# Performance work log

Hardware: AMD Instinct MI355X
Metric: run time of the kernel (lower is better)

Reference implementation:

```python
import jax, jax.numpy as jnp
import numpy as np

NEG_MASK_SCALE = -1e-09  # faithful to source (source uses -1e-09, likely intended -1e9)


def setup_inputs() -> dict:
    key0 = jax.random.key(0)
    ks = jax.random.split(key0, 7)
    B, Q, K, H = 4, 256, 1024, 128
    return {
        "query": jax.random.normal(ks[0], (B, Q, H), dtype=jnp.float32),
        "key": jax.random.normal(ks[1], (B, K, H), dtype=jnp.float32),
        "value": jax.random.normal(ks[2], (B, K, H), dtype=jnp.float32),
        "mask": jax.random.randint(ks[3], (B, Q, K), 0, 2).astype(jnp.int32),
        "Wq": jax.random.normal(ks[4], (H, H), dtype=jnp.float32) * (1.0 / np.sqrt(H)),
        "Wk": jax.random.normal(ks[5], (H, H), dtype=jnp.float32) * (1.0 / np.sqrt(H)),
        "v": jax.random.normal(ks[6], (H,), dtype=jnp.float32) * (1.0 / np.sqrt(H)),
    }


def reference(query, key, value, mask, Wq, Wk, v):
    # Projections: torch Linear computes x @ W.T
    q_proj = jnp.einsum("bqd,hd->bqh", query, Wq)  # (B, Q, H)
    k_proj = jnp.einsum("bkd,hd->bkh", key, Wk)    # (B, K, H)
    # Additive (Bahdanau) score: v . tanh(q_proj[:, :, None] + k_proj[:, None])
    feat = jnp.tanh(q_proj[:, :, None, :] + k_proj[:, None, :, :])  # (B, Q, K, H)
    score = jnp.einsum("bqkh,h->bqk", feat, v)                      # (B, Q, K)
    score = score + NEG_MASK_SCALE * (1.0 - mask.astype(score.dtype))
    attention_weights = jax.nn.softmax(score, axis=-1)              # (B, Q, K)
    context_vector = jnp.einsum("bqk,bkv->bqv", attention_weights, value)  # (B, Q, V)
    return attention_weights, context_vector
```

## Files before the change

### kernel.cpp

```cpp
#include <hip/hip_runtime.h>

#define Bb 4
#define Qn 256
#define Kn 1024
#define Hn 128

constexpr float SCALE = 2.88539008177792681f;

#if __has_builtin(__builtin_amdgcn_exp2f)
#define EXP2F(x) __builtin_amdgcn_exp2f(x)
#else
#define EXP2F(x) exp2f(x)
#endif
#if __has_builtin(__builtin_amdgcn_rcpf)
#define RCPF(x) __builtin_amdgcn_rcpf(x)
#else
#define RCPF(x) (1.0f / (x))
#endif

__global__ __launch_bounds__(128) void proj_kernel(const float* __restrict__ query,
                                                   const float* __restrict__ key,
                                                   const float* __restrict__ Wq,
                                                   const float* __restrict__ Wk,
                                                   float* __restrict__ eq,
                                                   float* __restrict__ ekT) {
    __shared__ float4 xs[128];
    const int tid = threadIdx.x;
    const bool isQ = blockIdx.x < (Bb * Qn / 4);
    const int r0 = (isQ ? blockIdx.x : blockIdx.x - Bb * Qn / 4) * 4;
    const float* x = isQ ? query : key;
    const float* W = isQ ? Wq : Wk;

    xs[tid] = ((const float4*)(x + (size_t)r0 * Hn))[tid];
    __syncthreads();
    const float4* W4 = (const float4*)W + (size_t)tid * (Hn / 4);
    float acc0 = 0.f, acc1 = 0.f, acc2 = 0.f, acc3 = 0.f;
#pragma unroll 8
    for (int d = 0; d < Hn / 4; ++d) {
        float4 w = W4[d];
        float4 a0 = xs[d];
        float4 a1 = xs[32 + d];
        float4 a2 = xs[64 + d];
        float4 a3 = xs[96 + d];
        acc0 = fmaf(w.x, a0.x, fmaf(w.y, a0.y, fmaf(w.z, a0.z, fmaf(w.w, a0.w, acc0))));
        acc1 = fmaf(w.x, a1.x, fmaf(w.y, a1.y, fmaf(w.z, a1.z, fmaf(w.w, a1.w, acc1))));
        acc2 = fmaf(w.x, a2.x, fmaf(w.y, a2.y, fmaf(w.z, a2.z, fmaf(w.w, a2.w, acc2))));
        acc3 = fmaf(w.x, a3.x, fmaf(w.y, a3.y, fmaf(w.z, a3.z, fmaf(w.w, a3.w, acc3))));
    }
    if (isQ) {
        eq[(size_t)(r0 + 0) * Hn + tid] = EXP2F(acc0 * SCALE);
        eq[(size_t)(r0 + 1) * Hn + tid] = EXP2F(acc1 * SCALE);
        eq[(size_t)(r0 + 2) * Hn + tid] = EXP2F(acc2 * SCALE);
        eq[(size_t)(r0 + 3) * Hn + tid] = EXP2F(acc3 * SCALE);
    } else {
        const int b = r0 / Kn;
        const int k0 = r0 % Kn;
        float4 res = make_float4(EXP2F(acc0 * SCALE), EXP2F(acc1 * SCALE),
                                 EXP2F(acc2 * SCALE), EXP2F(acc3 * SCALE));
        ((float4*)ekT)[((size_t)b * Hn + tid) * (Kn / 4) + (k0 >> 2)] = res;
    }
}

__global__ __launch_bounds__(1024) void score_softmax_kernel(const float* __restrict__ eq,
                                                             const float* __restrict__ ekT,
                                                             const float* __restrict__ v,
                                                             float* __restrict__ attn) {
    const int k = threadIdx.x;
    const int q = blockIdx.x;
    const int b = blockIdx.y;

    __shared__ float red[16][2];

    const float* eqrow = eq + ((size_t)b * Qn + q) * Hn;
    const float* ekb = ekT + (size_t)b * Hn * Kn + k;

    float a = 0.f;
#pragma unroll 16
    for (int h = 0; h < Hn; ++h) {
        const float qe = eqrow[h];
        const float vh = v[h];
        const float kv = ekb[(size_t)h * Kn];
        const float r = RCPF(fmaf(qe, kv, 1.0f));
        a = fmaf(vh, r, a);
    }

    const int lane = k & 63, wv = k >> 6;
    float mn = a;
#pragma unroll
    for (int off = 32; off; off >>= 1) mn = fminf(mn, __shfl_xor(mn, off));
    if (lane == 0) red[wv][0] = mn;
    __syncthreads();
    mn = red[0][0];
#pragma unroll
    for (int w = 1; w < 16; ++w) mn = fminf(mn, red[w][0]);

    const float e = EXP2F((mn - a) * SCALE);
    float s = e;
#pragma unroll
    for (int off = 32; off; off >>= 1) s += __shfl_xor(s, off);
    if (lane == 0) red[wv][1] = s;
    __syncthreads();
    s = red[0][1];
#pragma unroll
    for (int w = 1; w < 16; ++w) s += red[w][1];

    attn[((size_t)b * Qn + q) * Kn + k] = e * RCPF(s);
}

__global__ __launch_bounds__(1024) void ctx_kernel(const float* __restrict__ attn,
                                                   const float* __restrict__ value,
                                                   float* __restrict__ ctx) {
    const int tid = threadIdx.x;
    const int q0 = blockIdx.x * 4;
    const int b = blockIdx.y;

    __shared__ __align__(16) float4 pl[8][4][Hn / 4];

    const int kc = tid >> 7;
    const int cq = (tid >> 5) & 3;
    const int h4 = tid & 31;
    const float4* vb = (const float4*)(value + ((size_t)b * Kn + kc * 128) * Hn) + h4;
    const float* wr = attn + ((size_t)b * Qn + q0 + cq) * Kn + kc * 128;
    float4 acc = make_float4(0.f, 0.f, 0.f, 0.f);
#pragma unroll 4
    for (int kk = 0; kk < 128; ++kk) {
        const float wgt = wr[kk];
        const float4 vv = vb[(size_t)kk * (Hn / 4)];
        acc.x = fmaf(wgt, vv.x, acc.x);
        acc.y = fmaf(wgt, vv.y, acc.y);
        acc.z = fmaf(wgt, vv.z, acc.z);
        acc.w = fmaf(wgt, vv.w, acc.w);
    }
    pl[kc][cq][h4] = acc;
    __syncthreads();
    if (tid < 128) {
        const int q = tid >> 5, h = tid & 31;
        float4 r0 = pl[0][q][h], r1 = pl[1][q][h], r2 = pl[2][q][h], r3 = pl[3][q][h];
        float4 r4 = pl[4][q][h], r5 = pl[5][q][h], r6 = pl[6][q][h], r7 = pl[7][q][h];
        float4 sum;
        sum.x = ((r0.x + r1.x) + (r2.x + r3.x)) + ((r4.x + r5.x) + (r6.x + r7.x));
        sum.y = ((r0.y + r1.y) + (r2.y + r3.y)) + ((r4.y + r5.y) + (r6.y + r7.y));
        sum.z = ((r0.z + r1.z) + (r2.z + r3.z)) + ((r4.z + r5.z) + (r6.z + r7.z));
        sum.w = ((r0.w + r1.w) + (r2.w + r3.w)) + ((r4.w + r5.w) + (r6.w + r7.w));
        ((float4*)(ctx + ((size_t)b * Qn + q0 + q) * Hn))[h] = sum;
    }
}

extern "C" void kernel_launch(void* const* d_in, const int* in_sizes, int n_in,
                              void* d_out, int out_size, void* d_ws, size_t ws_size,
                              hipStream_t stream) {
    const float* query = (const float*)d_in[0];
    const float* key = (const float*)d_in[1];
    const float* value = (const float*)d_in[2];
    const float* Wq = (const float*)d_in[4];
    const float* Wk = (const float*)d_in[5];
    const float* v = (const float*)d_in[6];

    float* out = (float*)d_out;
    float* attn = out;
    float* ctx = out + (size_t)Bb * Qn * Kn;

    float* ws = (float*)d_ws;
    float* eq = ws;
    float* ekT = ws + 131072;

    proj_kernel<<<dim3(Bb * Qn / 4 + Bb * Kn / 4), dim3(128), 0, stream>>>(
        query, key, Wq, Wk, eq, ekT);
    score_softmax_kernel<<<dim3(Qn, Bb), dim3(1024), 0, stream>>>(
        eq, ekT, v, attn);
    ctx_kernel<<<dim3(Qn / 4, Bb), dim3(1024), 0, stream>>>(
        attn, value, ctx);
}
```

Before: 130.1 us.

## Split score and softmax kernels, register-tile four queries per thread

The fused score+softmax kernel is split into a score kernel and a separate softmax kernel. The score kernel now computes four query rows per thread over 256-key tiles, holding 64 key-exp values in registers, so each key load is reused across four queries instead of one. The cost is an extra kernel launch and a round trip of the full score matrix through workspace memory. Register pressure also rises from the 64-entry array.

```diff
diff --git a/kernel.cpp b/kernel.cpp
--- a/kernel.cpp
+++ b/kernel.cpp
@@ -61,28 +61,55 @@
     }
 }
 
-__global__ __launch_bounds__(1024) void score_softmax_kernel(const float* __restrict__ eq,
-                                                             const float* __restrict__ ekT,
-                                                             const float* __restrict__ v,
-                                                             float* __restrict__ attn) {
+__global__ __launch_bounds__(256) void score_kernel(const float* __restrict__ eq,
+                                                    const float* __restrict__ ekT,
+                                                    const float* __restrict__ v,
+                                                    float* __restrict__ scores) {
+    const int tid = threadIdx.x;
+    const int q0 = blockIdx.x * 4;
+    const int kc = blockIdx.y;
+    const int b = blockIdx.z;
+    const int k = kc * 256 + tid;
+
+    const float* ekb = ekT + (size_t)b * Hn * Kn + k;
+    const float* eqb = eq + ((size_t)b * Qn + q0) * Hn;
+
+    float a0 = 0.f, a1 = 0.f, a2 = 0.f, a3 = 0.f;
+    float ek[64];
+
+#pragma unroll
+    for (int half = 0; half < 2; ++half) {
+        const int hb = half * 64;
+#pragma unroll
+        for (int j = 0; j < 64; ++j) ek[j] = ekb[(size_t)(hb + j) * Kn];
+#pragma unroll
+        for (int j = 0; j < 64; ++j) {
+            const float vh = v[hb + j];
+            const float e = ek[j];
+            float r;
+            r = RCPF(fmaf(eqb[0 * Hn + hb + j], e, 1.0f)); a0 = fmaf(vh, r, a0);
+            r = RCPF(fmaf(eqb[1 * Hn + hb + j], e, 1.0f)); a1 = fmaf(vh, r, a1);
+            r = RCPF(fmaf(eqb[2 * Hn + hb + j], e, 1.0f)); a2 = fmaf(vh, r, a2);
+            r = RCPF(fmaf(eqb[3 * Hn + hb + j], e, 1.0f)); a3 = fmaf(vh, r, a3);
+        }
+    }
+
+    float* srow = scores + ((size_t)b * Qn + q0) * Kn + k;
+    srow[0 * Kn] = a0;
+    srow[1 * Kn] = a1;
+    srow[2 * Kn] = a2;
+    srow[3 * Kn] = a3;
+}
+
+__global__ __launch_bounds__(1024) void softmax_kernel(const float* __restrict__ scores,
+                                                       float* __restrict__ attn) {
     const int k = threadIdx.x;
     const int q = blockIdx.x;
     const int b = blockIdx.y;
 
     __shared__ float red[16][2];
 
-    const float* eqrow = eq + ((size_t)b * Qn + q) * Hn;
-    const float* ekb = ekT + (size_t)b * Hn * Kn + k;
-
-    float a = 0.f;
-#pragma unroll 16
-    for (int h = 0; h < Hn; ++h) {
-        const float qe = eqrow[h];
-        const float vh = v[h];
-        const float kv = ekb[(size_t)h * Kn];
-        const float r = RCPF(fmaf(qe, kv, 1.0f));
-        a = fmaf(vh, r, a);
-    }
+    const float a = scores[((size_t)b * Qn + q) * Kn + k];
 
     const int lane = k & 63, wv = k >> 6;
     float mn = a;
@@ -163,11 +190,12 @@
     float* ws = (float*)d_ws;
     float* eq = ws;
     float* ekT = ws + 131072;
+    float* scores = ws + 131072 + 524288;
 
     proj_kernel<<<dim3(Bb * Qn / 4 + Bb * Kn / 4), dim3(128), 0, stream>>>(
         query, key, Wq, Wk, eq, ekT);
-    score_softmax_kernel<<<dim3(Qn, Bb), dim3(1024), 0, stream>>>(
-        eq, ekT, v, attn);
-    ctx_kernel<<<dim3(Qn / 4, Bb), dim3(1024), 0, stream>>>(
-        attn, value, ctx);
-}
+    score_kernel<<<dim3(Qn / 4, Kn / 256, Bb), dim3(256), 0, stream>>>(
+        eq, ekT, v, scores);
+    softmax_kernel<<<dim3(Qn, Bb), dim3(1024), 0, stream>>>(scores, attn);
+    ctx_kernel<<<dim3(Qn / 4, Bb), dim3(1024), 0, stream>>>(attn, value, ctx);
+}
```

After: 129.8 us. Within noise of the previous version (-0.3%).
